# Kernel tuning notes

Measured on AMD Instinct MI355X. Metric: run time of the kernel, lower is better.

The kernel has to match this reference:

```python
import jax, jax.numpy as jnp
import numpy as np
import math

B, S, DIM, QK, HID = 20, 500, 300, 128, 600  # batch, seq, model dim, query_key_dim, hidden_dim
ROT = 32          # rotary dim = min(32, query_key_dim)
NB, MD = 32, 128  # T5 bias num_buckets, max_distance


def _layernorm(x, g, b, eps=1e-5):
    mu = jnp.mean(x, axis=-1, keepdims=True)
    var = jnp.var(x, axis=-1, keepdims=True)
    return (x - mu) / jnp.sqrt(var + eps) * g + b


def _rowquant(y, axis):
    # per-row (or per-col) symmetric int4-range quant used by the module:
    # scale = max|y|/15, clamp to [-15,15], truncate toward zero (torch .to(int8))
    s = jnp.max(jnp.abs(y), axis=axis, keepdims=True) / 15.0
    yq = jnp.trunc(jnp.clip(y / s, -15.0, 15.0))
    return yq, s


def _rotary(t):
    # rotary-embedding-torch: rotate first ROT features, interleaved pairs
    inv_freq = 1.0 / (10000.0 ** (jnp.arange(0, ROT, 2, dtype=jnp.float32) / ROT))  # [ROT/2]
    pos = jnp.arange(S, dtype=jnp.float32)
    freqs = jnp.repeat(pos[:, None] * inv_freq[None, :], 2, axis=-1)  # [S, ROT]
    cos, sin = jnp.cos(freqs), jnp.sin(freqs)
    tr, tp = t[..., :ROT], t[..., ROT:]
    x1, x2 = tr[..., 0::2], tr[..., 1::2]
    rot_half = jnp.stack([-x2, x1], axis=-1).reshape(tr.shape)
    return jnp.concatenate([tr * cos + rot_half * sin, tp], axis=-1)


def _t5_bias(rel_emb):
    # non-causal T5 relative position bucket, num_buckets=32 -> halved to 16
    pos = jnp.arange(S)
    n = -(pos[None, :] - pos[:, None])  # -(k_pos - q_pos)
    nb = NB // 2
    ret = (n < 0).astype(jnp.int32) * nb
    n = jnp.abs(n)
    max_exact = nb // 2
    is_small = n < max_exact
    n_safe = jnp.maximum(n, 1).astype(jnp.float32)
    val_large = max_exact + (jnp.log(n_safe / max_exact) / math.log(MD / max_exact) * (nb - max_exact)).astype(jnp.int32)
    val_large = jnp.minimum(val_large, nb - 1)
    bucket = ret + jnp.where(is_small, n, val_large)  # [S, S]
    return rel_emb[bucket, 0] * math.sqrt(QK)


def setup_inputs() -> dict:
    key = jax.random.key(0)
    ks = jax.random.split(key, 16)
    nrm = lambda i, shp, std=0.02: jax.random.normal(ks[i], shp, jnp.float32) * std
    uni = lambda i, shp, lo, hi: jax.random.uniform(ks[i], shp, jnp.float32, lo, hi)
    return {
        "x": jax.random.normal(ks[0], (B, S, DIM), jnp.float32),
        "norm_gamma": jnp.ones((DIM,), jnp.float32),
        "norm_beta": jnp.zeros((DIM,), jnp.float32),
        "Wh": nrm(1, (2 * HID, DIM)),
        "bh": jnp.zeros((2 * HID,), jnp.float32),
        "Wqk": nrm(2, (QK, DIM)),
        "bqk": jnp.zeros((QK,), jnp.float32),
        "os_gamma": nrm(3, (2, QK)),
        "os_beta": jnp.zeros((2, QK), jnp.float32),
        "Wo": nrm(4, (DIM, HID)),
        "bo": jnp.zeros((DIM,), jnp.float32),
        "rel_emb": nrm(5, (NB, 1), 0.1),
        "qk_s": uni(6, (DIM,), 0.5, 1.5),
        "hidden_s": uni(7, (DIM,), 0.5, 1.5),
        "out_s": uni(8, (HID,), 0.5, 1.5),
        "hidden_params": uni(9, (2 * HID,), 0.01, 0.05),
        "qk_params": uni(10, (QK,), 0.01, 0.05),
        "out_params": uni(11, (DIM,), 0.01, 0.05),
    }


def reference(x, norm_gamma, norm_beta, Wh, bh, Wqk, bqk, os_gamma, os_beta, Wo, bo,
              rel_emb, qk_s, hidden_s, out_s, hidden_params, qk_params, out_params):
    normed = _layernorm(x, norm_gamma, norm_beta)
    # token shift on first half of features
    half = DIM // 2
    x_shift = jnp.pad(normed[..., :half], ((0, 0), (1, 0), (0, 0)))[:, :S, :]
    normed = jnp.concatenate([x_shift, normed[..., half:]], axis=-1)

    # per-weight-column pre-scale then per-row int8 quant
    xq_q, sq = _rowquant(normed / qk_s, axis=-1)      # sq [B,S,1]
    xh_q, sh = _rowquant(normed / hidden_s, axis=-1)  # sh [B,S,1]

    # to_hidden: Linear + SiLU, then dequant outer(row_scale, hidden_params)
    v_gate = jax.nn.silu(xh_q @ Wh.T + bh) * (sh * hidden_params)  # [B,S,2*HID]
    v, gate = v_gate[..., :HID], v_gate[..., HID:]

    qk = jax.nn.silu(xq_q @ Wqk.T + bqk) * (sq * qk_params)  # [B,S,QK]
    q = qk * os_gamma[0] + os_beta[0]
    k = qk * os_gamma[1] + os_beta[1]
    q, k = _rotary(q), _rotary(k)

    qq, qs = _rowquant(q, axis=-1)
    kq, ks_ = _rowquant(k, axis=-1)
    sim = jnp.trunc(jnp.einsum('bid,bjd->bij', qq, kq)) * qs * jnp.swapaxes(ks_, 1, 2)
    sim = sim + _t5_bias(rel_emb)

    attn = jnp.square(jax.nn.relu(sim / S))
    aq, as_ = _rowquant(attn, axis=-1)  # as_ [B,S,1]
    vq, vs = _rowquant(v, axis=1)       # vs [B,1,HID] (per-column)
    out = jnp.trunc(jnp.einsum('bij,bjd->bid', aq, vq)) * as_ * vs  # [B,S,HID]

    out = out * gate / out_s
    oq, osc = _rowquant(out, axis=-1)
    out = (oq @ Wo.T + bo) * (osc * out_params)  # [B,S,DIM]
    return out + x
```

## Files before the change

kernel.cpp:

```cpp
#include <hip/hip_runtime.h>
#include <math.h>

#define B_   20
#define S_   500
#define DIM_ 300
#define QK_  128
#define HID_ 600
#define NROW (B_ * S_)

typedef int   v4i  __attribute__((ext_vector_type(4)));

__device__ __forceinline__ unsigned short f32_to_bf16(float f) {
  unsigned int u = __float_as_uint(f);
  unsigned int r = (u + 0x7FFFu + ((u >> 16) & 1u)) >> 16;
  return (unsigned short)r;
}
__device__ __forceinline__ float bf16_to_f32(unsigned short s) {
  return __uint_as_float(((unsigned int)s) << 16);
}

__device__ __forceinline__ float quant15(float y, float s) {
  return truncf(fminf(fmaxf(__fdiv_rn(y, s), -15.f), 15.f));
}

__global__ __launch_bounds__(64) void k_prep(
    const float* __restrict__ rel_emb, float* __restrict__ dbias,
    const float* __restrict__ Wh, signed char* __restrict__ q1h, float* __restrict__ s1h,
    const float* __restrict__ Wo, signed char* __restrict__ q1o,
    signed char* __restrict__ q2o, float* __restrict__ s1o, float* __restrict__ s2o,
    const float* __restrict__ Wqk, signed char* __restrict__ q1k,
    signed char* __restrict__ q2k, float* __restrict__ s1k, float* __restrict__ s2k) {
  __shared__ float red[64];
  int blk = blockIdx.x;
  int tid = threadIdx.x;
  if (blk < 16) {
    int idx = blk * 64 + tid;
    int dd = idx - 512;
    int ret = (dd < 0) ? 16 : 0;
    int n = dd < 0 ? -dd : dd;
    int v;
    if (n < 8)       v = n;
    else if (n < 12) v = 8;
    else if (n < 16) v = 9;
    else if (n < 23) v = 10;
    else if (n < 32) v = 11;
    else if (n < 46) v = 12;
    else if (n < 64) v = 13;
    else if (n < 91) v = 14;
    else             v = 15;
    dbias[idx] = __fmul_rn(rel_emb[ret + v], 11.313708498984761f);
    return;
  }
  const float* src; signed char* q1; signed char* q2; float* s1; float* s2;
  int j, R, C, CP;
  bool twolevel;
  if (blk < 1296) {
    j = blk - 16;  src = Wh;  q1 = q1h; q2 = 0; s1 = s1h; s2 = 0;
    R = 2 * HID_; C = DIM_; CP = 320; twolevel = false;
  } else if (blk < 1616) {
    j = blk - 1296; src = Wo; q1 = q1o; q2 = q2o; s1 = s1o; s2 = s2o;
    R = DIM_; C = HID_; CP = 640; twolevel = true;
  } else {
    j = blk - 1616; src = Wqk; q1 = q1k; q2 = q2k; s1 = s1k; s2 = s2k;
    R = QK_; C = DIM_; CP = 320; twolevel = true;
  }
  float m = 0.f;
  if (j < R)
    for (int k = tid; k < C; k += 64) m = fmaxf(m, fabsf(src[(size_t)j * C + k]));
  red[tid] = m; __syncthreads();
  for (int off = 32; off > 0; off >>= 1) {
    if (tid < off) red[tid] = fmaxf(red[tid], red[tid + off]);
    __syncthreads();
  }
  float s1v = red[0] / 127.0f;
  float s1inv = s1v > 0.f ? 1.0f / s1v : 0.f;
  if (!twolevel) {
    if (tid == 0) s1[j] = s1v;
    for (int k = tid; k < CP; k += 64) {
      float wv = (j < R && k < C) ? src[(size_t)j * C + k] : 0.f;
      float q1f = fminf(fmaxf(rintf(wv * s1inv), -127.f), 127.f);
      q1[(size_t)j * CP + k] = (signed char)q1f;
    }
    return;
  }
  __syncthreads();
  float mr = 0.f;
  if (j < R)
    for (int k = tid; k < C; k += 64) {
      float wv = src[(size_t)j * C + k];
      float q = fminf(fmaxf(rintf(wv * s1inv), -127.f), 127.f);
      mr = fmaxf(mr, fabsf(wv - s1v * q));
    }
  red[tid] = mr; __syncthreads();
  for (int off = 32; off > 0; off >>= 1) {
    if (tid < off) red[tid] = fmaxf(red[tid], red[tid + off]);
    __syncthreads();
  }
  float s2v = red[0] / 127.0f;
  float s2inv = s2v > 0.f ? 1.0f / s2v : 0.f;
  if (tid == 0) { s1[j] = s1v; s2[j] = s2v; }
  for (int k = tid; k < CP; k += 64) {
    float wv = (j < R && k < C) ? src[(size_t)j * C + k] : 0.f;
    float q1f = fminf(fmaxf(rintf(wv * s1inv), -127.f), 127.f);
    float rs = wv - s1v * q1f;
    float q2f = fminf(fmaxf(rintf(rs * s2inv), -127.f), 127.f);
    q1[(size_t)j * CP + k] = (signed char)q1f;
    q2[(size_t)j * CP + k] = (signed char)q2f;
  }
}

__global__ __launch_bounds__(256) void k_lnshift(
    const float* __restrict__ x,
    const float* __restrict__ g, const float* __restrict__ b,
    const float* __restrict__ qk_s, const float* __restrict__ hidden_s,
    signed char* __restrict__ xq8, signed char* __restrict__ xh8,
    float* __restrict__ sq, float* __restrict__ sh) {
  int lane = threadIdx.x & 63;
  int row = blockIdx.x * 4 + (threadIdx.x >> 6);
  if (row >= NROW) return;
  bool hasp = (row % S_) > 0;
  const float* xr = x + (size_t)row * DIM_;
  const float* xpr = x + (size_t)(row - 1) * DIM_;
  float xc[5], xp[5];
  #pragma unroll
  for (int i = 0; i < 5; ++i) {
    int c = lane + i * 64;
    xc[i] = (c < DIM_) ? xr[c] : 0.f;
    xp[i] = (hasp && c < DIM_) ? xpr[c] : 0.f;
  }
  float sc = 0.f, sp = 0.f;
  #pragma unroll
  for (int i = 0; i < 5; ++i) { sc += xc[i]; sp += xp[i]; }
  #pragma unroll
  for (int off = 1; off < 64; off <<= 1) {
    sc += __shfl_xor(sc, off);
    sp += __shfl_xor(sp, off);
  }
  float mu_c = sc / (float)DIM_, mu_p = sp / (float)DIM_;
  float vc = 0.f, vp = 0.f;
  #pragma unroll
  for (int i = 0; i < 5; ++i) {
    int c = lane + i * 64;
    if (c < DIM_) {
      float dc = xc[i] - mu_c; vc += dc * dc;
      float dp = xp[i] - mu_p; vp += dp * dp;
    }
  }
  #pragma unroll
  for (int off = 1; off < 64; off <<= 1) {
    vc += __shfl_xor(vc, off);
    vp += __shfl_xor(vp, off);
  }
  float den_c = sqrtf(vc / (float)DIM_ + 1e-5f);
  float den_p = sqrtf(vp / (float)DIM_ + 1e-5f);
  float yq[5], yh[5];
  float mq = 0.f, mh = 0.f;
  #pragma unroll
  for (int i = 0; i < 5; ++i) {
    int c = lane + i * 64;
    if (c < DIM_) {
      float src;
      if (c < DIM_ / 2)
        src = hasp ? __fdiv_rn(xp[i] - mu_p, den_p) * g[c] + b[c] : 0.f;
      else
        src = __fdiv_rn(xc[i] - mu_c, den_c) * g[c] + b[c];
      yq[i] = __fdiv_rn(src, qk_s[c]);
      yh[i] = __fdiv_rn(src, hidden_s[c]);
      mq = fmaxf(mq, fabsf(yq[i]));
      mh = fmaxf(mh, fabsf(yh[i]));
    }
  }
  #pragma unroll
  for (int off = 1; off < 64; off <<= 1) {
    mq = fmaxf(mq, __shfl_xor(mq, off));
    mh = fmaxf(mh, __shfl_xor(mh, off));
  }
  float sqv = mq / 15.0f, shv = mh / 15.0f;
  if (lane == 0) { sq[row] = sqv; sh[row] = shv; }
  #pragma unroll
  for (int i = 0; i < 5; ++i) {
    int c = lane + i * 64;
    if (c < DIM_) {
      xq8[(size_t)row * 320 + c] = (signed char)quant15(yq[i], sqv);
      xh8[(size_t)row * 320 + c] = (signed char)quant15(yh[i], shv);
    } else if (c < 320) {
      xq8[(size_t)row * 320 + c] = 0;
      xh8[(size_t)row * 320 + c] = 0;
    }
  }
}

__global__ __launch_bounds__(512) void k_hidden(
    const signed char* __restrict__ xh8p, const float* __restrict__ sh,
    const signed char* __restrict__ q1h, const float* __restrict__ s1h,
    const float* __restrict__ bh, const float* __restrict__ hp,
    unsigned short* __restrict__ v16, unsigned short* __restrict__ gate16,
    int* __restrict__ vsmax) {
  int i0 = blockIdx.y * 256;
  int j0 = blockIdx.x * 64;
  int tid = threadIdx.x;
  int w = tid >> 6, l = tid & 63, g = l >> 4, ln = l & 15;
  int wm = w >> 1, wn = w & 1;
  __shared__ __align__(16) signed char smem[33792];
  signed char* a_lds  = smem;
  signed char* b1_lds = smem + 16384;
  unsigned short* st  = (unsigned short*)smem;

  int r0 = tid >> 2, ch0 = tid & 3;
  int r1 = r0 + 128, ch1 = ch0;
  int koff0 = ((ch0 ^ ((r0 >> 1) & 3)) * 16);
  int koff1 = ((ch1 ^ ((r1 >> 1) & 3)) * 16);
  int ga0 = i0 + r0; if (ga0 >= NROW) ga0 = NROW - 1;
  int ga1 = i0 + r1; if (ga1 >= NROW) ga1 = NROW - 1;
  const signed char* srcA0 = xh8p + (size_t)ga0 * 320 + koff0;
  const signed char* srcA1 = xh8p + (size_t)ga1 * 320 + koff1;
  bool hasB = tid < 256;
  int br = (tid & 255) >> 2, bch = tid & 3;
  int bkoff = ((bch ^ ((br >> 1) & 3)) * 16);
  const signed char* srcB = q1h + (size_t)(j0 + br) * 320 + bkoff;

  v4i pa0 = *(const v4i*)srcA0;
  v4i pa1 = *(const v4i*)srcA1;
  v4i zero = {0, 0, 0, 0};
  v4i pb = hasB ? *(const v4i*)srcB : zero;

  int rxor = ((g ^ ((ln >> 1) & 3)) * 16);
  v4i acc1[4][2];
  #pragma unroll
  for (int sl = 0; sl < 4; ++sl)
    #pragma unroll
    for (int t = 0; t < 2; ++t) acc1[sl][t] = zero;

  for (int st_i = 0; st_i < 5; ++st_i) {
    *(v4i*)(a_lds + tid * 16)        = pa0;
    *(v4i*)(a_lds + 8192 + tid * 16) = pa1;
    if (hasB) *(v4i*)(b1_lds + tid * 16) = pb;
    __syncthreads();
    if (st_i < 4) {
      int k0 = (st_i + 1) * 64;
      pa0 = *(const v4i*)(srcA0 + k0);
      pa1 = *(const v4i*)(srcA1 + k0);
      if (hasB) pb = *(const v4i*)(srcB + k0);
    }
    v4i af[4];
    #pragma unroll
    for (int sl = 0; sl < 4; ++sl)
      af[sl] = *(const v4i*)(a_lds + (wm * 64 + sl * 16 + ln) * 64 + rxor);
    #pragma unroll
    for (int t = 0; t < 2; ++t) {
      int boff = (wn * 32 + t * 16 + ln) * 64 + rxor;
      v4i b1 = *(const v4i*)(b1_lds + boff);
      #pragma unroll
      for (int sl = 0; sl < 4; ++sl)
        acc1[sl][t] = __builtin_amdgcn_mfma_i32_16x16x64_i8(af[sl], b1, acc1[sl][t], 0, 0, 0);
    }
    __syncthreads();
  }
  int rbase = i0 + wm * 64;
  int b0 = rbase / S_;
  int bbound = (b0 + 1) * S_;
  int rtop = rbase + 63; if (rtop >= NROW) rtop = NROW - 1;
  int b1i = rtop / S_;
  #pragma unroll
  for (int t = 0; t < 2; ++t) {
    int col = j0 + wn * 32 + t * 16 + ln;
    int cl = wn * 32 + t * 16 + ln;
    if (col < 2 * HID_) {
      float s1v = s1h[col], bc = bh[col], hpc = hp[col];
      bool isv = col < HID_;
      float m0 = 0.f, m1 = 0.f;
      #pragma unroll
      for (int sl = 0; sl < 4; ++sl) {
        #pragma unroll
        for (int r = 0; r < 4; ++r) {
          int grow = rbase + sl * 16 + g * 4 + r;
          if (grow < NROW) {
            float z = s1v * (float)acc1[sl][t][r] + bc;
            float sig = 1.0f / (1.0f + __expf(-z));
            float val = __fmul_rn(z * sig, __fmul_rn(sh[grow], hpc));
            unsigned short hv = f32_to_bf16(val);
            st[(wm * 64 + sl * 16 + g * 4 + r) * 66 + cl] = hv;
            if (isv) {
              float vr = fabsf(bf16_to_f32(hv));
              if (grow < bbound) m0 = fmaxf(m0, vr);
              else               m1 = fmaxf(m1, vr);
            }
          }
        }
      }
      if (isv) {
        atomicMax(&vsmax[b0 * 640 + col], __float_as_int(m0));
        if (b1i != b0) atomicMax(&vsmax[b1i * 640 + col], __float_as_int(m1));
      }
    }
  }
  __syncthreads();
  for (int idx = tid; idx < 2048; idx += 512) {
    int r = idx >> 3, seg = idx & 7;
    int grow = i0 + r;
    int col0 = j0 + seg * 8;
    if (grow < NROW && col0 < 2 * HID_) {
      const unsigned int* sp = (const unsigned int*)(st + r * 66 + seg * 8);
      v4i pk;
      pk[0] = sp[0]; pk[1] = sp[1]; pk[2] = sp[2]; pk[3] = sp[3];
      if (col0 < HID_)
        *(v4i*)(v16 + (size_t)grow * HID_ + col0) = pk;
      else
        *(v4i*)(gate16 + (size_t)grow * HID_ + (col0 - HID_)) = pk;
    }
  }
}

__global__ __launch_bounds__(256) void k_qk(
    const signed char* __restrict__ xq8p, const float* __restrict__ sq,
    const signed char* __restrict__ q1k, const signed char* __restrict__ q2k,
    const float* __restrict__ s1k, const float* __restrict__ s2k,
    const float* __restrict__ bqk, const float* __restrict__ qkp,
    const float* __restrict__ osg, const float* __restrict__ osb,
    signed char* __restrict__ qq8, signed char* __restrict__ kq2,
    float* __restrict__ qs, float* __restrict__ ks) {
  int i0 = blockIdx.x * 64;
  int tid = threadIdx.x;
  int w = tid >> 6, l = tid & 63, g = l >> 4, ln = l & 15;
  __shared__ __align__(16) signed char a_lds[64 * 64];
  __shared__ __align__(16) signed char b1_lds[128 * 64];
  __shared__ __align__(16) signed char b2_lds[128 * 64];
  __shared__ float freqs[32];
  if (tid < 32) {
    double e = (double)(tid & ~1) / 32.0;
    freqs[tid] = (float)(1.0 / pow(10000.0, e));
  }
  int arow = tid >> 2;
  int xorb = (((tid & 3) ^ ((tid >> 3) & 3)) * 16);
  int ga = i0 + arow; if (ga >= NROW) ga = NROW - 1;
  const signed char* srcA   = xq8p + (size_t)ga * 320 + xorb;
  const signed char* srcB1a = q1k + (size_t)arow * 320 + xorb;
  const signed char* srcB1b = q1k + (size_t)(64 + arow) * 320 + xorb;
  const signed char* srcB2a = q2k + (size_t)arow * 320 + xorb;
  const signed char* srcB2b = q2k + (size_t)(64 + arow) * 320 + xorb;
  v4i pa   = *(const v4i*)srcA;
  v4i pb1a = *(const v4i*)srcB1a, pb1b = *(const v4i*)srcB1b;
  v4i pb2a = *(const v4i*)srcB2a, pb2b = *(const v4i*)srcB2b;
  int rxor = ((g ^ ((ln >> 1) & 3)) * 16);
  v4i acc1[8], acc2[8];
  v4i zero = {0, 0, 0, 0};
  #pragma unroll
  for (int t = 0; t < 8; ++t) { acc1[t] = zero; acc2[t] = zero; }
  for (int st = 0; st < 5; ++st) {
    *(v4i*)(a_lds + tid * 16)         = pa;
    *(v4i*)(b1_lds + tid * 16)        = pb1a;
    *(v4i*)(b1_lds + 4096 + tid * 16) = pb1b;
    *(v4i*)(b2_lds + tid * 16)        = pb2a;
    *(v4i*)(b2_lds + 4096 + tid * 16) = pb2b;
    __syncthreads();
    if (st < 4) {
      int k0 = (st + 1) * 64;
      pa   = *(const v4i*)(srcA + k0);
      pb1a = *(const v4i*)(srcB1a + k0);
      pb1b = *(const v4i*)(srcB1b + k0);
      pb2a = *(const v4i*)(srcB2a + k0);
      pb2b = *(const v4i*)(srcB2b + k0);
    }
    v4i af = *(const v4i*)(a_lds + (w * 16 + ln) * 64 + rxor);
    #pragma unroll
    for (int t = 0; t < 8; ++t) {
      int boff = (t * 16 + ln) * 64 + rxor;
      v4i b1 = *(const v4i*)(b1_lds + boff);
      v4i b2 = *(const v4i*)(b2_lds + boff);
      acc1[t] = __builtin_amdgcn_mfma_i32_16x16x64_i8(af, b1, acc1[t], 0, 0, 0);
      acc2[t] = __builtin_amdgcn_mfma_i32_16x16x64_i8(af, b2, acc2[t], 0, 0, 0);
    }
    __syncthreads();
  }
  int growr[4]; float sqr[4];
  #pragma unroll
  for (int r = 0; r < 4; ++r) {
    growr[r] = i0 + w * 16 + g * 4 + r;
    int gc = growr[r] < NROW ? growr[r] : NROW - 1;
    sqr[r] = sq[gc];
  }
  float qv[8][4], kv[8][4];
  #pragma unroll
  for (int t = 0; t < 8; ++t) {
    int c = t * 16 + ln;
    float s1v = s1k[c], s2v = s2k[c], bc = bqk[c], qkpc = qkp[c];
    float g0 = osg[c], g1 = osg[QK_ + c], b0 = osb[c], b1v = osb[QK_ + c];
    #pragma unroll
    for (int r = 0; r < 4; ++r) {
      float z = s1v * (float)acc1[t][r] + s2v * (float)acc2[t][r] + bc;
      float sig = 1.0f / (1.0f + expf(-z));
      float qkv = __fmul_rn(z * sig, __fmul_rn(sqr[r], qkpc));
      qv[t][r] = __fadd_rn(__fmul_rn(qkv, g0), b0);
      kv[t][r] = __fadd_rn(__fmul_rn(qkv, g1), b1v);
    }
  }
  #pragma unroll
  for (int t = 0; t < 2; ++t) {
    float inv = freqs[t * 16 + ln];
    #pragma unroll
    for (int r = 0; r < 4; ++r) {
      int pos = growr[r] % S_;
      float fr = __fmul_rn((float)pos, inv);
      float cs = cosf(fr), sn = sinf(fr);
      float qo = __shfl_xor(qv[t][r], 1);
      float ko = __shfl_xor(kv[t][r], 1);
      float rq = ((ln & 1) == 0) ? -qo : qo;
      float rk = ((ln & 1) == 0) ? -ko : ko;
      qv[t][r] = __fadd_rn(__fmul_rn(qv[t][r], cs), __fmul_rn(rq, sn));
      kv[t][r] = __fadd_rn(__fmul_rn(kv[t][r], cs), __fmul_rn(rk, sn));
    }
  }
  float qsv[4], ksv[4];
  #pragma unroll
  for (int r = 0; r < 4; ++r) {
    float mq = 0.f, mk = 0.f;
    #pragma unroll
    for (int t = 0; t < 8; ++t) {
      mq = fmaxf(mq, fabsf(qv[t][r]));
      mk = fmaxf(mk, fabsf(kv[t][r]));
    }
    #pragma unroll
    for (int off = 1; off < 16; off <<= 1) {
      mq = fmaxf(mq, __shfl_xor(mq, off));
      mk = fmaxf(mk, __shfl_xor(mk, off));
    }
    qsv[r] = mq / 15.0f; ksv[r] = mk / 15.0f;
    if (ln == 0 && growr[r] < NROW) { qs[growr[r]] = qsv[r]; ks[growr[r]] = ksv[r]; }
  }
  #pragma unroll
  for (int t = 0; t < 8; ++t) {
    int c = t * 16 + ln;
    #pragma unroll
    for (int r = 0; r < 4; ++r) {
      if (growr[r] < NROW) {
        qq8[(size_t)growr[r] * QK_ + c] = (signed char)quant15(qv[t][r], qsv[r]);
        int bb = growr[r] / S_, ss = growr[r] % S_;
        kq2[(((size_t)bb * 2 + (c >> 6)) * 512 + ss) * 64 + (c & 63)] =
            (signed char)quant15(kv[t][r], ksv[r]);
      }
    }
  }
}

__global__ __launch_bounds__(512) void k_simpv(
    const signed char* __restrict__ qq8, const signed char* __restrict__ kq2,
    const float* __restrict__ qs, const float* __restrict__ ks,
    const float* __restrict__ dbias,
    const signed char* __restrict__ vqt2, const float* __restrict__ vg,
    const unsigned short* __restrict__ gate16,
    signed char* __restrict__ oq8, float* __restrict__ osc) {
  int i0 = blockIdx.x * 16;
  int b = blockIdx.y;
  int tid = threadIdx.x;
  int w = tid >> 6, l = tid & 63, g = l >> 4, ln = l & 15;
  __shared__ __align__(16) signed char q_lds[16 * 144];
  __shared__ __align__(16) signed char p_lds[16 * 528];
  __shared__ float db[1024];
  __shared__ int rowmax[16];
  if (tid < 128) {
    int r = tid >> 3, ww = tid & 7;
    *(v4i*)(q_lds + r * 144 + ww * 16) =
        *(const v4i*)(qq8 + ((size_t)(b * S_ + i0 + r)) * QK_ + ww * 16);
  }
  for (int idx = tid; idx < 1024; idx += 512) db[idx] = dbias[idx];
  if (tid < 16) rowmax[tid] = 0;
  __syncthreads();
  v4i acc[4];
  v4i zero = {0, 0, 0, 0};
  #pragma unroll
  for (int t = 0; t < 4; ++t) acc[t] = zero;
  #pragma unroll
  for (int kk = 0; kk < 2; ++kk) {
    v4i afrag = *(const v4i*)(q_lds + ln * 144 + kk * 64 + g * 16);
    #pragma unroll
    for (int t = 0; t < 4; ++t) {
      int j0 = (w * 4 + t) * 16;
      v4i bfrag = *(const v4i*)(kq2 + (((size_t)b * 2 + kk) * 512 + j0 + ln) * 64 + g * 16);
      acc[t] = __builtin_amdgcn_mfma_i32_16x16x64_i8(afrag, bfrag, acc[t], 0, 0, 0);
    }
  }
  float qsr[4];
  #pragma unroll
  for (int r = 0; r < 4; ++r) qsr[r] = qs[b * S_ + i0 + g * 4 + r];
  float rm[4] = {0.f, 0.f, 0.f, 0.f};
  #pragma unroll
  for (int t = 0; t < 4; ++t) {
    int j = (w * 4 + t) * 16 + ln;
    bool jv = j < S_;
    float ksv = ks[b * S_ + j];
    #pragma unroll
    for (int r = 0; r < 4; ++r) {
      int ip = i0 + g * 4 + r;
      float av = 0.f;
      if (jv) {
        float simv = __fmul_rn(__fmul_rn((float)acc[t][r], qsr[r]), ksv);
        simv = __fadd_rn(simv, db[ip - j + 512]);
        float rr = fmaxf(__fmul_rn(simv, 0.002f), 0.f);
        av = __fmul_rn(rr, rr);
      }
      rm[r] = fmaxf(rm[r], av);
      acc[t][r] = __float_as_int(av);
    }
  }
  #pragma unroll
  for (int r = 0; r < 4; ++r) atomicMax(&rowmax[g * 4 + r], __float_as_int(rm[r]));
  __syncthreads();
  float asr[4], rinv[4];
  #pragma unroll
  for (int r = 0; r < 4; ++r) {
    asr[r] = __int_as_float(rowmax[g * 4 + r]) / 15.0f;
    rinv[r] = __fdiv_rn(1.0f, asr[r]);
  }
  #pragma unroll
  for (int t = 0; t < 4; ++t) {
    int j = (w * 4 + t) * 16 + ln;
    #pragma unroll
    for (int r = 0; r < 4; ++r) {
      float y = __int_as_float(acc[t][r]);
      float q = truncf(fminf(fmaxf(__fmul_rn(y, rinv[r]), -15.f), 15.f));
      p_lds[(g * 4 + r) * 528 + j] = (signed char)q;
    }
  }
  __syncthreads();
  if (tid < 16) rowmax[tid] = 0;
  __syncthreads();
  v4i pacc[5];
  #pragma unroll
  for (int t = 0; t < 5; ++t) pacc[t] = zero;
  for (int kk = 0; kk < 8; ++kk) {
    v4i afrag = *(const v4i*)(p_lds + ln * 528 + kk * 64 + g * 16);
    const signed char* bbase = vqt2 + (((size_t)b * 8 + kk) * 640) * 64 + g * 16;
    #pragma unroll
    for (int t = 0; t < 5; ++t) {
      int d = (w * 5 + t) * 16 + ln;
      v4i bfrag = *(const v4i*)(bbase + (size_t)d * 64);
      pacc[t] = __builtin_amdgcn_mfma_i32_16x16x64_i8(afrag, bfrag, pacc[t], 0, 0, 0);
    }
  }
  float rm2[4] = {0.f, 0.f, 0.f, 0.f};
  #pragma unroll
  for (int t = 0; t < 5; ++t) {
    int d = (w * 5 + t) * 16 + ln;
    bool dv = d < HID_;
    float vgv = vg[b * 640 + d];
    #pragma unroll
    for (int r = 0; r < 4; ++r) {
      float o = 0.f;
      if (dv) {
        float gt = bf16_to_f32(gate16[((size_t)(b * S_ + i0 + g * 4 + r)) * HID_ + d]);
        o = __fmul_rn(__fmul_rn(__fmul_rn((float)pacc[t][r], asr[r]), vgv), gt);
      }
      rm2[r] = fmaxf(rm2[r], fabsf(o));
      pacc[t][r] = __float_as_int(o);
    }
  }
  #pragma unroll
  for (int r = 0; r < 4; ++r) atomicMax(&rowmax[g * 4 + r], __float_as_int(rm2[r]));
  __syncthreads();
  float orinv[4];
  #pragma unroll
  for (int r = 0; r < 4; ++r) {
    float osr = __int_as_float(rowmax[g * 4 + r]) / 15.0f;
    orinv[r] = __fdiv_rn(1.0f, osr);
  }
  #pragma unroll
  for (int t = 0; t < 5; ++t) {
    int d = (w * 5 + t) * 16 + ln;
    #pragma unroll
    for (int r = 0; r < 4; ++r) {
      int il = i0 + g * 4 + r;
      if (il < S_) {
        signed char valc = 0;
        if (d < HID_) {
          float q = truncf(fminf(fmaxf(
              __fmul_rn(__int_as_float(pacc[t][r]), orinv[r]), -15.f), 15.f));
          valc = (signed char)q;
        }
        oq8[((size_t)b * S_ + il) * 640 + d] = valc;
      }
    }
  }
  if (tid < 16 && i0 + tid < S_)
    osc[b * S_ + i0 + tid] = __int_as_float(rowmax[tid]) / 15.0f;
}

__global__ __launch_bounds__(256) void k_vq2(const unsigned short* __restrict__ v16,
                                             const int* __restrict__ vsmax,
                                             const float* __restrict__ out_s,
                                             signed char* __restrict__ vqt2,
                                             float* __restrict__ vg) {
  int b = blockIdx.z;
  int s0 = blockIdx.x * 64;
  int d0 = blockIdx.y * 64;
  __shared__ float tile[64][65];
  int tid = threadIdx.x;
  int dj = tid & 63, si4 = tid >> 6;
  #pragma unroll
  for (int it = 0; it < 16; ++it) {
    int s = s0 + it * 4 + si4;
    int d = d0 + dj;
    float val = 0.f;
    if (s < S_ && d < HID_) val = bf16_to_f32(v16[((size_t)b * S_ + s) * HID_ + d]);
    tile[it * 4 + si4][dj] = val;
  }
  if (blockIdx.x == 0 && tid < 64) {
    int d = d0 + tid;
    float vsv = __int_as_float(vsmax[b * 640 + d]) / 15.0f;
    vg[b * 640 + d] = (d < HID_) ? __fdiv_rn(vsv, out_s[d]) : 0.f;
  }
  __syncthreads();
  int dd = tid >> 2, seg = tid & 3;
  int d = d0 + dd;
  int kk = s0 >> 6;
  v4i pack = {0, 0, 0, 0};
  if (d < HID_) {
    float vsv = __int_as_float(vsmax[b * 640 + d]) / 15.0f;
    signed char* pc = (signed char*)&pack;
    #pragma unroll
    for (int e = 0; e < 16; ++e)
      pc[e] = (signed char)quant15(tile[seg * 16 + e][dd], vsv);
  }
  *(v4i*)(vqt2 + ((((size_t)b * 8 + kk) * 640) + d) * 64 + seg * 16) = pack;
}

__global__ __launch_bounds__(256) void k_final(
    const signed char* __restrict__ oq8p, const float* __restrict__ osc,
    const signed char* __restrict__ q1o, const signed char* __restrict__ q2o,
    const float* __restrict__ s1o, const float* __restrict__ s2o,
    const float* __restrict__ bo, const float* __restrict__ op,
    const float* __restrict__ x, float* __restrict__ out) {
  int i0 = blockIdx.x * 128;
  int j0 = blockIdx.y * 64;
  int tid = threadIdx.x;
  int w = tid >> 6, l = tid & 63, g = l >> 4, ln = l & 15;
  int wm = w >> 1, wn = w & 1;
  __shared__ __align__(16) signed char a_lds[128 * 64];
  __shared__ __align__(16) signed char b1_lds[64 * 64];
  __shared__ __align__(16) signed char b2_lds[64 * 64];

  int arow0 = tid >> 2;
  int xorb = (((tid & 3) ^ ((tid >> 3) & 3)) * 16);
  int ga0 = i0 + arow0;       if (ga0 >= NROW) ga0 = NROW - 1;
  int ga1 = i0 + arow0 + 64;  if (ga1 >= NROW) ga1 = NROW - 1;
  int gcol = j0 + arow0;
  const signed char* srcA0 = oq8p + (size_t)ga0 * 640 + xorb;
  const signed char* srcA1 = oq8p + (size_t)ga1 * 640 + xorb;
  const signed char* srcB1 = q1o + (size_t)gcol * 640 + xorb;
  const signed char* srcB2 = q2o + (size_t)gcol * 640 + xorb;

  v4i pa0 = *(const v4i*)(srcA0);
  v4i pa1 = *(const v4i*)(srcA1);
  v4i pb1 = *(const v4i*)(srcB1);
  v4i pb2 = *(const v4i*)(srcB2);

  int rxor = ((g ^ ((ln >> 1) & 3)) * 16);
  v4i acc1[4][2], acc2[4][2];
  v4i zero = {0, 0, 0, 0};
  #pragma unroll
  for (int sl = 0; sl < 4; ++sl)
    #pragma unroll
    for (int t = 0; t < 2; ++t) { acc1[sl][t] = zero; acc2[sl][t] = zero; }

  for (int st = 0; st < 10; ++st) {
    *(v4i*)(a_lds + tid * 16)        = pa0;
    *(v4i*)(a_lds + 4096 + tid * 16) = pa1;
    *(v4i*)(b1_lds + tid * 16)       = pb1;
    *(v4i*)(b2_lds + tid * 16)       = pb2;
    __syncthreads();
    if (st < 9) {
      int k0 = (st + 1) * 64;
      pa0 = *(const v4i*)(srcA0 + k0);
      pa1 = *(const v4i*)(srcA1 + k0);
      pb1 = *(const v4i*)(srcB1 + k0);
      pb2 = *(const v4i*)(srcB2 + k0);
    }
    v4i af[4];
    #pragma unroll
    for (int sl = 0; sl < 4; ++sl)
      af[sl] = *(const v4i*)(a_lds + (wm * 64 + sl * 16 + ln) * 64 + rxor);
    #pragma unroll
    for (int t = 0; t < 2; ++t) {
      int boff = (wn * 32 + t * 16 + ln) * 64 + rxor;
      v4i b1 = *(const v4i*)(b1_lds + boff);
      v4i b2 = *(const v4i*)(b2_lds + boff);
      #pragma unroll
      for (int sl = 0; sl < 4; ++sl) {
        acc1[sl][t] = __builtin_amdgcn_mfma_i32_16x16x64_i8(af[sl], b1, acc1[sl][t], 0, 0, 0);
        acc2[sl][t] = __builtin_amdgcn_mfma_i32_16x16x64_i8(af[sl], b2, acc2[sl][t], 0, 0, 0);
      }
    }
    __syncthreads();
  }
  #pragma unroll
  for (int t = 0; t < 2; ++t) {
    int col = j0 + wn * 32 + t * 16 + ln;
    if (col < DIM_) {
      float s1v = s1o[col], s2v = s2o[col], bc = bo[col], opc = op[col];
      #pragma unroll
      for (int sl = 0; sl < 4; ++sl) {
        #pragma unroll
        for (int r = 0; r < 4; ++r) {
          int grow = i0 + wm * 64 + sl * 16 + g * 4 + r;
          if (grow < NROW) {
            float z = s1v * (float)acc1[sl][t][r] + s2v * (float)acc2[sl][t][r] + bc;
            float tval = __fmul_rn(osc[grow], opc);
            out[(size_t)grow * DIM_ + col] =
                __fmul_rn(z, tval) + x[(size_t)grow * DIM_ + col];
          }
        }
      }
    }
  }
}

extern "C" void kernel_launch(void* const* d_in, const int* in_sizes, int n_in,
                              void* d_out, int out_size, void* d_ws, size_t ws_size,
                              hipStream_t stream) {
  const float* x        = (const float*)d_in[0];
  const float* ng       = (const float*)d_in[1];
  const float* nbt      = (const float*)d_in[2];
  const float* Wh       = (const float*)d_in[3];
  const float* bh       = (const float*)d_in[4];
  const float* Wqk      = (const float*)d_in[5];
  const float* bqk      = (const float*)d_in[6];
  const float* osg      = (const float*)d_in[7];
  const float* osb      = (const float*)d_in[8];
  const float* Wo       = (const float*)d_in[9];
  const float* bo       = (const float*)d_in[10];
  const float* rel      = (const float*)d_in[11];
  const float* qk_s     = (const float*)d_in[12];
  const float* hidden_s = (const float*)d_in[13];
  const float* out_s    = (const float*)d_in[14];
  const float* hp       = (const float*)d_in[15];
  const float* qkp      = (const float*)d_in[16];
  const float* op       = (const float*)d_in[17];
  float* out = (float*)d_out;

  char* ws = (char*)d_ws;
  size_t off = 0;
  auto alloc = [&](size_t bytes) {
    void* p = ws + off;
    off += (bytes + 255) & ~(size_t)255;
    return p;
  };
  signed char* xq8    = (signed char*)alloc((size_t)(NROW + 128) * 320);
  signed char* xh8    = (signed char*)alloc((size_t)(NROW + 256) * 320);
  float*       sq     = (float*)      alloc((size_t)(NROW + 256) * 4);
  float*       sh     = (float*)      alloc((size_t)(NROW + 256) * 4);
  unsigned short* v16   = (unsigned short*)alloc((size_t)(NROW + 256) * HID_ * 2);
  unsigned short* gate16= (unsigned short*)alloc((size_t)(NROW + 256) * HID_ * 2);
  signed char* qq8    = (signed char*)alloc((size_t)(NROW + 64) * QK_);
  signed char* kq2    = (signed char*)alloc((size_t)B_ * 2 * 512 * 64);
  float*       qs     = (float*)      alloc((size_t)(NROW + 64) * 4);
  float*       ks     = (float*)      alloc((size_t)(NROW + 64) * 4);
  signed char* vqt2   = (signed char*)alloc((size_t)B_ * 8 * 640 * 64);
  float*       vg     = (float*)      alloc((size_t)B_ * 640 * 4);
  int*         vsmax  = (int*)        alloc((size_t)B_ * 640 * 4);
  signed char* oq8    = (signed char*)alloc((size_t)(NROW + 128) * 640);
  float*       osc    = (float*)      alloc((size_t)(NROW + 128) * 4);
  float*       dbias  = (float*)      alloc((size_t)1024 * 4);
  signed char* q1h    = (signed char*)alloc((size_t)1280 * 320);
  float*       s1h    = (float*)      alloc((size_t)1280 * 4);
  signed char* q1o    = (signed char*)alloc((size_t)320 * 640);
  signed char* q2o    = (signed char*)alloc((size_t)320 * 640);
  float*       s1o    = (float*)      alloc((size_t)320 * 4);
  float*       s2o    = (float*)      alloc((size_t)320 * 4);
  signed char* q1k    = (signed char*)alloc((size_t)QK_ * 320);
  signed char* q2k    = (signed char*)alloc((size_t)QK_ * 320);
  float*       s1k    = (float*)      alloc((size_t)QK_ * 4);
  float*       s2k    = (float*)      alloc((size_t)QK_ * 4);


  k_prep<<<1744, 64, 0, stream>>>(rel, dbias, Wh, q1h, s1h,
                                  Wo, q1o, q2o, s1o, s2o,
                                  Wqk, q1k, q2k, s1k, s2k);
  k_lnshift<<<(NROW + 3) / 4, 256, 0, stream>>>(x, ng, nbt, qk_s, hidden_s, xq8, xh8, sq, sh);
  k_hidden<<<dim3(19, 40), 512, 0, stream>>>(xh8, sh, q1h, s1h, bh, hp,
                                             v16, gate16, vsmax);
  k_qk<<<157, 256, 0, stream>>>(xq8, sq, q1k, q2k, s1k, s2k, bqk, qkp, osg, osb,
                                qq8, kq2, qs, ks);
  k_vq2<<<dim3(8, 10, B_), 256, 0, stream>>>(v16, vsmax, out_s, vqt2, vg);
  k_simpv<<<dim3(32, B_), 512, 0, stream>>>(qq8, kq2, qs, ks, dbias, vqt2, vg,
                                            gate16, oq8, osc);
  k_final<<<dim3(79, 5), 256, 0, stream>>>(oq8, osc, q1o, q2o, s1o, s2o, bo, op, x, out);
}
```

Baseline: 135.7 us.

## Fuse prep with layernorm, hidden with qk GEMM, and drop Wo residual quant

```diff
diff --git a/kernel.cpp b/kernel.cpp
--- a/kernel.cpp
+++ b/kernel.cpp
@@ -23,18 +23,99 @@
   return truncf(fminf(fmaxf(__fdiv_rn(y, s), -15.f), 15.f));
 }
 
-__global__ __launch_bounds__(64) void k_prep(
+__global__ __launch_bounds__(256) void k_prep_ln(
+    const float* __restrict__ x,
+    const float* __restrict__ g, const float* __restrict__ b,
+    const float* __restrict__ qk_s, const float* __restrict__ hidden_s,
+    signed char* __restrict__ xq8, signed char* __restrict__ xh8,
+    float* __restrict__ sq, float* __restrict__ sh,
     const float* __restrict__ rel_emb, float* __restrict__ dbias,
     const float* __restrict__ Wh, signed char* __restrict__ q1h, float* __restrict__ s1h,
-    const float* __restrict__ Wo, signed char* __restrict__ q1o,
-    signed char* __restrict__ q2o, float* __restrict__ s1o, float* __restrict__ s2o,
+    const float* __restrict__ Wo, signed char* __restrict__ q1o, float* __restrict__ s1o,
     const float* __restrict__ Wqk, signed char* __restrict__ q1k,
     signed char* __restrict__ q2k, float* __restrict__ s1k, float* __restrict__ s2k) {
-  __shared__ float red[64];
   int blk = blockIdx.x;
   int tid = threadIdx.x;
-  if (blk < 16) {
-    int idx = blk * 64 + tid;
+  int lane = tid & 63;
+  if (blk < 2500) {
+    int row = blk * 4 + (tid >> 6);
+    if (row >= NROW) return;
+    bool hasp = (row % S_) > 0;
+    const float* xr = x + (size_t)row * DIM_;
+    const float* xpr = x + (size_t)(row - 1) * DIM_;
+    float xc[5], xp[5];
+    #pragma unroll
+    for (int i = 0; i < 5; ++i) {
+      int c = lane + i * 64;
+      xc[i] = (c < DIM_) ? xr[c] : 0.f;
+      xp[i] = (hasp && c < DIM_) ? xpr[c] : 0.f;
+    }
+    float sc = 0.f, sp = 0.f;
+    #pragma unroll
+    for (int i = 0; i < 5; ++i) { sc += xc[i]; sp += xp[i]; }
+    #pragma unroll
+    for (int off = 1; off < 64; off <<= 1) {
+      sc += __shfl_xor(sc, off);
+      sp += __shfl_xor(sp, off);
+    }
+    float mu_c = sc / (float)DIM_, mu_p = sp / (float)DIM_;
+    float vc = 0.f, vp = 0.f;
+    #pragma unroll
+    for (int i = 0; i < 5; ++i) {
+      int c = lane + i * 64;
+      if (c < DIM_) {
+        float dc = xc[i] - mu_c; vc += dc * dc;
+        float dp = xp[i] - mu_p; vp += dp * dp;
+      }
+    }
+    #pragma unroll
+    for (int off = 1; off < 64; off <<= 1) {
+      vc += __shfl_xor(vc, off);
+      vp += __shfl_xor(vp, off);
+    }
+    float den_c = sqrtf(vc / (float)DIM_ + 1e-5f);
+    float den_p = sqrtf(vp / (float)DIM_ + 1e-5f);
+    float yq[5], yh[5];
+    float mq = 0.f, mh = 0.f;
+    #pragma unroll
+    for (int i = 0; i < 5; ++i) {
+      int c = lane + i * 64;
+      if (c < DIM_) {
+        float src;
+        if (c < DIM_ / 2)
+          src = hasp ? __fdiv_rn(xp[i] - mu_p, den_p) * g[c] + b[c] : 0.f;
+        else
+          src = __fdiv_rn(xc[i] - mu_c, den_c) * g[c] + b[c];
+        yq[i] = __fdiv_rn(src, qk_s[c]);
+        yh[i] = __fdiv_rn(src, hidden_s[c]);
+        mq = fmaxf(mq, fabsf(yq[i]));
+        mh = fmaxf(mh, fabsf(yh[i]));
+      }
+    }
+    #pragma unroll
+    for (int off = 1; off < 64; off <<= 1) {
+      mq = fmaxf(mq, __shfl_xor(mq, off));
+      mh = fmaxf(mh, __shfl_xor(mh, off));
+    }
+    float sqv = mq / 15.0f, shv = mh / 15.0f;
+    if (lane == 0) { sq[row] = sqv; sh[row] = shv; }
+    #pragma unroll
+    for (int i = 0; i < 5; ++i) {
+      int c = lane + i * 64;
+      if (c < DIM_) {
+        xq8[(size_t)row * 320 + c] = (signed char)quant15(yq[i], sqv);
+        xh8[(size_t)row * 320 + c] = (signed char)quant15(yh[i], shv);
+      } else if (c < 320) {
+        xq8[(size_t)row * 320 + c] = 0;
+        xh8[(size_t)row * 320 + c] = 0;
+      }
+    }
+    return;
+  }
+  int jidx = (blk - 2500) * 4 + (tid >> 6);
+  if (jidx >= 1744) return;
+  if (jidx < 16) {
+    int idx = jidx * 64 + lane;
     int dd = idx - 512;
     int ret = (dd < 0) ? 16 : 0;
     int n = dd < 0 ? -dd : dd;
@@ -51,392 +132,289 @@
     dbias[idx] = __fmul_rn(rel_emb[ret + v], 11.313708498984761f);
     return;
   }
-  const float* src; signed char* q1; signed char* q2; float* s1; float* s2;
-  int j, R, C, CP;
+  const float* src; signed char* q1; float* s1;
+  int j, C, CP;
   bool twolevel;
-  if (blk < 1296) {
-    j = blk - 16;  src = Wh;  q1 = q1h; q2 = 0; s1 = s1h; s2 = 0;
-    R = 2 * HID_; C = DIM_; CP = 320; twolevel = false;
-  } else if (blk < 1616) {
-    j = blk - 1296; src = Wo; q1 = q1o; q2 = q2o; s1 = s1o; s2 = s2o;
-    R = DIM_; C = HID_; CP = 640; twolevel = true;
-  } else {
-    j = blk - 1616; src = Wqk; q1 = q1k; q2 = q2k; s1 = s1k; s2 = s2k;
-    R = QK_; C = DIM_; CP = 320; twolevel = true;
-  }
+  if (jidx < 1296)      { j = jidx - 16;   src = Wh;  q1 = q1h; s1 = s1h; C = DIM_; CP = 320; twolevel = false; }
+  else if (jidx < 1616) { j = jidx - 1296; src = Wo;  q1 = q1o; s1 = s1o; C = HID_; CP = 640; twolevel = false; }
+  else                  { j = jidx - 1616; src = Wqk; q1 = q1k; s1 = s1k; C = DIM_; CP = 320; twolevel = true;  }
   float m = 0.f;
-  if (j < R)
-    for (int k = tid; k < C; k += 64) m = fmaxf(m, fabsf(src[(size_t)j * C + k]));
-  red[tid] = m; __syncthreads();
-  for (int off = 32; off > 0; off >>= 1) {
-    if (tid < off) red[tid] = fmaxf(red[tid], red[tid + off]);
-    __syncthreads();
-  }
-  float s1v = red[0] / 127.0f;
+  for (int k = lane; k < C; k += 64) m = fmaxf(m, fabsf(src[(size_t)j * C + k]));
+  #pragma unroll
+  for (int off = 1; off < 64; off <<= 1) m = fmaxf(m, __shfl_xor(m, off));
+  float s1v = m / 127.0f;
   float s1inv = s1v > 0.f ? 1.0f / s1v : 0.f;
   if (!twolevel) {
-    if (tid == 0) s1[j] = s1v;
-    for (int k = tid; k < CP; k += 64) {
-      float wv = (j < R && k < C) ? src[(size_t)j * C + k] : 0.f;
+    if (lane == 0) s1[j] = s1v;
+    for (int k = lane; k < CP; k += 64) {
+      float wv = (k < C) ? src[(size_t)j * C + k] : 0.f;
       float q1f = fminf(fmaxf(rintf(wv * s1inv), -127.f), 127.f);
       q1[(size_t)j * CP + k] = (signed char)q1f;
     }
     return;
   }
-  __syncthreads();
   float mr = 0.f;
-  if (j < R)
-    for (int k = tid; k < C; k += 64) {
-      float wv = src[(size_t)j * C + k];
-      float q = fminf(fmaxf(rintf(wv * s1inv), -127.f), 127.f);
-      mr = fmaxf(mr, fabsf(wv - s1v * q));
-    }
-  red[tid] = mr; __syncthreads();
-  for (int off = 32; off > 0; off >>= 1) {
-    if (tid < off) red[tid] = fmaxf(red[tid], red[tid + off]);
-    __syncthreads();
-  }
-  float s2v = red[0] / 127.0f;
+  for (int k = lane; k < C; k += 64) {
+    float wv = src[(size_t)j * C + k];
+    float q = fminf(fmaxf(rintf(wv * s1inv), -127.f), 127.f);
+    mr = fmaxf(mr, fabsf(wv - s1v * q));
+  }
+  #pragma unroll
+  for (int off = 1; off < 64; off <<= 1) mr = fmaxf(mr, __shfl_xor(mr, off));
+  float s2v = mr / 127.0f;
   float s2inv = s2v > 0.f ? 1.0f / s2v : 0.f;
-  if (tid == 0) { s1[j] = s1v; s2[j] = s2v; }
-  for (int k = tid; k < CP; k += 64) {
-    float wv = (j < R && k < C) ? src[(size_t)j * C + k] : 0.f;
+  if (lane == 0) { s1k[j] = s1v; s2k[j] = s2v; }
+  for (int k = lane; k < CP; k += 64) {
+    float wv = (k < C) ? src[(size_t)j * C + k] : 0.f;
     float q1f = fminf(fmaxf(rintf(wv * s1inv), -127.f), 127.f);
     float rs = wv - s1v * q1f;
     float q2f = fminf(fmaxf(rintf(rs * s2inv), -127.f), 127.f);
-    q1[(size_t)j * CP + k] = (signed char)q1f;
-    q2[(size_t)j * CP + k] = (signed char)q2f;
-  }
-}
-
-__global__ __launch_bounds__(256) void k_lnshift(
-    const float* __restrict__ x,
-    const float* __restrict__ g, const float* __restrict__ b,
-    const float* __restrict__ qk_s, const float* __restrict__ hidden_s,
-    signed char* __restrict__ xq8, signed char* __restrict__ xh8,
-    float* __restrict__ sq, float* __restrict__ sh) {
-  int lane = threadIdx.x & 63;
-  int row = blockIdx.x * 4 + (threadIdx.x >> 6);
-  if (row >= NROW) return;
-  bool hasp = (row % S_) > 0;
-  const float* xr = x + (size_t)row * DIM_;
-  const float* xpr = x + (size_t)(row - 1) * DIM_;
-  float xc[5], xp[5];
-  #pragma unroll
-  for (int i = 0; i < 5; ++i) {
-    int c = lane + i * 64;
-    xc[i] = (c < DIM_) ? xr[c] : 0.f;
-    xp[i] = (hasp && c < DIM_) ? xpr[c] : 0.f;
-  }
-  float sc = 0.f, sp = 0.f;
-  #pragma unroll
-  for (int i = 0; i < 5; ++i) { sc += xc[i]; sp += xp[i]; }
-  #pragma unroll
-  for (int off = 1; off < 64; off <<= 1) {
-    sc += __shfl_xor(sc, off);
-    sp += __shfl_xor(sp, off);
-  }
-  float mu_c = sc / (float)DIM_, mu_p = sp / (float)DIM_;
-  float vc = 0.f, vp = 0.f;
-  #pragma unroll
-  for (int i = 0; i < 5; ++i) {
-    int c = lane + i * 64;
-    if (c < DIM_) {
-      float dc = xc[i] - mu_c; vc += dc * dc;
-      float dp = xp[i] - mu_p; vp += dp * dp;
-    }
-  }
-  #pragma unroll
-  for (int off = 1; off < 64; off <<= 1) {
-    vc += __shfl_xor(vc, off);
-    vp += __shfl_xor(vp, off);
-  }
-  float den_c = sqrtf(vc / (float)DIM_ + 1e-5f);
-  float den_p = sqrtf(vp / (float)DIM_ + 1e-5f);
-  float yq[5], yh[5];
-  float mq = 0.f, mh = 0.f;
-  #pragma unroll
-  for (int i = 0; i < 5; ++i) {
-    int c = lane + i * 64;
-    if (c < DIM_) {
-      float src;
-      if (c < DIM_ / 2)
-        src = hasp ? __fdiv_rn(xp[i] - mu_p, den_p) * g[c] + b[c] : 0.f;
-      else
-        src = __fdiv_rn(xc[i] - mu_c, den_c) * g[c] + b[c];
-      yq[i] = __fdiv_rn(src, qk_s[c]);
-      yh[i] = __fdiv_rn(src, hidden_s[c]);
-      mq = fmaxf(mq, fabsf(yq[i]));
-      mh = fmaxf(mh, fabsf(yh[i]));
-    }
-  }
-  #pragma unroll
-  for (int off = 1; off < 64; off <<= 1) {
-    mq = fmaxf(mq, __shfl_xor(mq, off));
-    mh = fmaxf(mh, __shfl_xor(mh, off));
-  }
-  float sqv = mq / 15.0f, shv = mh / 15.0f;
-  if (lane == 0) { sq[row] = sqv; sh[row] = shv; }
-  #pragma unroll
-  for (int i = 0; i < 5; ++i) {
-    int c = lane + i * 64;
-    if (c < DIM_) {
-      xq8[(size_t)row * 320 + c] = (signed char)quant15(yq[i], sqv);
-      xh8[(size_t)row * 320 + c] = (signed char)quant15(yh[i], shv);
-    } else if (c < 320) {
-      xq8[(size_t)row * 320 + c] = 0;
-      xh8[(size_t)row * 320 + c] = 0;
-    }
-  }
-}
-
-__global__ __launch_bounds__(512) void k_hidden(
-    const signed char* __restrict__ xh8p, const float* __restrict__ sh,
+    q1k[(size_t)j * CP + k] = (signed char)q1f;
+    q2k[(size_t)j * CP + k] = (signed char)q2f;
+  }
+}
+
+__global__ __launch_bounds__(512) void k_hqk(
+    const signed char* __restrict__ xh8p, const signed char* __restrict__ xq8p,
+    const float* __restrict__ sh, const float* __restrict__ sq,
     const signed char* __restrict__ q1h, const float* __restrict__ s1h,
     const float* __restrict__ bh, const float* __restrict__ hp,
     unsigned short* __restrict__ v16, unsigned short* __restrict__ gate16,
-    int* __restrict__ vsmax) {
-  int i0 = blockIdx.y * 256;
-  int j0 = blockIdx.x * 64;
-  int tid = threadIdx.x;
-  int w = tid >> 6, l = tid & 63, g = l >> 4, ln = l & 15;
-  int wm = w >> 1, wn = w & 1;
-  __shared__ __align__(16) signed char smem[33792];
-  signed char* a_lds  = smem;
-  signed char* b1_lds = smem + 16384;
-  unsigned short* st  = (unsigned short*)smem;
-
-  int r0 = tid >> 2, ch0 = tid & 3;
-  int r1 = r0 + 128, ch1 = ch0;
-  int koff0 = ((ch0 ^ ((r0 >> 1) & 3)) * 16);
-  int koff1 = ((ch1 ^ ((r1 >> 1) & 3)) * 16);
-  int ga0 = i0 + r0; if (ga0 >= NROW) ga0 = NROW - 1;
-  int ga1 = i0 + r1; if (ga1 >= NROW) ga1 = NROW - 1;
-  const signed char* srcA0 = xh8p + (size_t)ga0 * 320 + koff0;
-  const signed char* srcA1 = xh8p + (size_t)ga1 * 320 + koff1;
-  bool hasB = tid < 256;
-  int br = (tid & 255) >> 2, bch = tid & 3;
-  int bkoff = ((bch ^ ((br >> 1) & 3)) * 16);
-  const signed char* srcB = q1h + (size_t)(j0 + br) * 320 + bkoff;
-
-  v4i pa0 = *(const v4i*)srcA0;
-  v4i pa1 = *(const v4i*)srcA1;
-  v4i zero = {0, 0, 0, 0};
-  v4i pb = hasB ? *(const v4i*)srcB : zero;
-
-  int rxor = ((g ^ ((ln >> 1) & 3)) * 16);
-  v4i acc1[4][2];
-  #pragma unroll
-  for (int sl = 0; sl < 4; ++sl)
-    #pragma unroll
-    for (int t = 0; t < 2; ++t) acc1[sl][t] = zero;
-
-  for (int st_i = 0; st_i < 5; ++st_i) {
-    *(v4i*)(a_lds + tid * 16)        = pa0;
-    *(v4i*)(a_lds + 8192 + tid * 16) = pa1;
-    if (hasB) *(v4i*)(b1_lds + tid * 16) = pb;
-    __syncthreads();
-    if (st_i < 4) {
-      int k0 = (st_i + 1) * 64;
-      pa0 = *(const v4i*)(srcA0 + k0);
-      pa1 = *(const v4i*)(srcA1 + k0);
-      if (hasB) pb = *(const v4i*)(srcB + k0);
-    }
-    v4i af[4];
-    #pragma unroll
-    for (int sl = 0; sl < 4; ++sl)
-      af[sl] = *(const v4i*)(a_lds + (wm * 64 + sl * 16 + ln) * 64 + rxor);
-    #pragma unroll
-    for (int t = 0; t < 2; ++t) {
-      int boff = (wn * 32 + t * 16 + ln) * 64 + rxor;
-      v4i b1 = *(const v4i*)(b1_lds + boff);
-      #pragma unroll
-      for (int sl = 0; sl < 4; ++sl)
-        acc1[sl][t] = __builtin_amdgcn_mfma_i32_16x16x64_i8(af[sl], b1, acc1[sl][t], 0, 0, 0);
-    }
-    __syncthreads();
-  }
-  int rbase = i0 + wm * 64;
-  int b0 = rbase / S_;
-  int bbound = (b0 + 1) * S_;
-  int rtop = rbase + 63; if (rtop >= NROW) rtop = NROW - 1;
-  int b1i = rtop / S_;
-  #pragma unroll
-  for (int t = 0; t < 2; ++t) {
-    int col = j0 + wn * 32 + t * 16 + ln;
-    int cl = wn * 32 + t * 16 + ln;
-    if (col < 2 * HID_) {
-      float s1v = s1h[col], bc = bh[col], hpc = hp[col];
-      bool isv = col < HID_;
-      float m0 = 0.f, m1 = 0.f;
-      #pragma unroll
-      for (int sl = 0; sl < 4; ++sl) {
-        #pragma unroll
-        for (int r = 0; r < 4; ++r) {
-          int grow = rbase + sl * 16 + g * 4 + r;
-          if (grow < NROW) {
-            float z = s1v * (float)acc1[sl][t][r] + bc;
-            float sig = 1.0f / (1.0f + __expf(-z));
-            float val = __fmul_rn(z * sig, __fmul_rn(sh[grow], hpc));
-            unsigned short hv = f32_to_bf16(val);
-            st[(wm * 64 + sl * 16 + g * 4 + r) * 66 + cl] = hv;
-            if (isv) {
-              float vr = fabsf(bf16_to_f32(hv));
-              if (grow < bbound) m0 = fmaxf(m0, vr);
-              else               m1 = fmaxf(m1, vr);
-            }
-          }
-        }
-      }
-      if (isv) {
-        atomicMax(&vsmax[b0 * 640 + col], __float_as_int(m0));
-        if (b1i != b0) atomicMax(&vsmax[b1i * 640 + col], __float_as_int(m1));
-      }
-    }
-  }
-  __syncthreads();
-  for (int idx = tid; idx < 2048; idx += 512) {
-    int r = idx >> 3, seg = idx & 7;
-    int grow = i0 + r;
-    int col0 = j0 + seg * 8;
-    if (grow < NROW && col0 < 2 * HID_) {
-      const unsigned int* sp = (const unsigned int*)(st + r * 66 + seg * 8);
-      v4i pk;
-      pk[0] = sp[0]; pk[1] = sp[1]; pk[2] = sp[2]; pk[3] = sp[3];
-      if (col0 < HID_)
-        *(v4i*)(v16 + (size_t)grow * HID_ + col0) = pk;
-      else
-        *(v4i*)(gate16 + (size_t)grow * HID_ + (col0 - HID_)) = pk;
-    }
-  }
-}
-
-__global__ __launch_bounds__(256) void k_qk(
-    const signed char* __restrict__ xq8p, const float* __restrict__ sq,
+    int* __restrict__ vsmax,
     const signed char* __restrict__ q1k, const signed char* __restrict__ q2k,
     const float* __restrict__ s1k, const float* __restrict__ s2k,
     const float* __restrict__ bqk, const float* __restrict__ qkp,
     const float* __restrict__ osg, const float* __restrict__ osb,
     signed char* __restrict__ qq8, signed char* __restrict__ kq2,
     float* __restrict__ qs, float* __restrict__ ks) {
-  int i0 = blockIdx.x * 64;
+  __shared__ __align__(16) signed char smem[33792];
+  int blk = blockIdx.x;
   int tid = threadIdx.x;
   int w = tid >> 6, l = tid & 63, g = l >> 4, ln = l & 15;
-  __shared__ __align__(16) signed char a_lds[64 * 64];
-  __shared__ __align__(16) signed char b1_lds[128 * 64];
-  __shared__ __align__(16) signed char b2_lds[128 * 64];
-  __shared__ float freqs[32];
-  if (tid < 32) {
-    double e = (double)(tid & ~1) / 32.0;
-    freqs[tid] = (float)(1.0 / pow(10000.0, e));
-  }
-  int arow = tid >> 2;
-  int xorb = (((tid & 3) ^ ((tid >> 3) & 3)) * 16);
-  int ga = i0 + arow; if (ga >= NROW) ga = NROW - 1;
-  const signed char* srcA   = xq8p + (size_t)ga * 320 + xorb;
-  const signed char* srcB1a = q1k + (size_t)arow * 320 + xorb;
-  const signed char* srcB1b = q1k + (size_t)(64 + arow) * 320 + xorb;
-  const signed char* srcB2a = q2k + (size_t)arow * 320 + xorb;
-  const signed char* srcB2b = q2k + (size_t)(64 + arow) * 320 + xorb;
-  v4i pa   = *(const v4i*)srcA;
-  v4i pb1a = *(const v4i*)srcB1a, pb1b = *(const v4i*)srcB1b;
-  v4i pb2a = *(const v4i*)srcB2a, pb2b = *(const v4i*)srcB2b;
+  v4i zero = {0, 0, 0, 0};
   int rxor = ((g ^ ((ln >> 1) & 3)) * 16);
-  v4i acc1[8], acc2[8];
-  v4i zero = {0, 0, 0, 0};
-  #pragma unroll
-  for (int t = 0; t < 8; ++t) { acc1[t] = zero; acc2[t] = zero; }
-  for (int st = 0; st < 5; ++st) {
-    *(v4i*)(a_lds + tid * 16)         = pa;
-    *(v4i*)(b1_lds + tid * 16)        = pb1a;
-    *(v4i*)(b1_lds + 4096 + tid * 16) = pb1b;
-    *(v4i*)(b2_lds + tid * 16)        = pb2a;
-    *(v4i*)(b2_lds + 4096 + tid * 16) = pb2b;
+
+  if (blk < 760) {
+    int j0 = (blk % 19) * 64;
+    int i0 = (blk / 19) * 256;
+    int wm = w >> 1, wn = w & 1;
+    signed char* a_lds  = smem;
+    signed char* b1_lds = smem + 16384;
+    unsigned short* st  = (unsigned short*)smem;
+
+    int r0 = tid >> 2, ch0 = tid & 3;
+    int r1 = r0 + 128;
+    int koff0 = ((ch0 ^ ((r0 >> 1) & 3)) * 16);
+    int koff1 = ((ch0 ^ ((r1 >> 1) & 3)) * 16);
+    int ga0 = i0 + r0; if (ga0 >= NROW) ga0 = NROW - 1;
+    int ga1 = i0 + r1; if (ga1 >= NROW) ga1 = NROW - 1;
+    const signed char* srcA0 = xh8p + (size_t)ga0 * 320 + koff0;
+    const signed char* srcA1 = xh8p + (size_t)ga1 * 320 + koff1;
+    bool hasB = tid < 256;
+    int br = (tid & 255) >> 2, bch = tid & 3;
+    int bkoff = ((bch ^ ((br >> 1) & 3)) * 16);
+    const signed char* srcB = q1h + (size_t)(j0 + br) * 320 + bkoff;
+
+    v4i pa0 = *(const v4i*)srcA0;
+    v4i pa1 = *(const v4i*)srcA1;
+    v4i pb = hasB ? *(const v4i*)srcB : zero;
+
+    v4i acc1[4][2];
+    #pragma unroll
+    for (int sl = 0; sl < 4; ++sl)
+      #pragma unroll
+      for (int t = 0; t < 2; ++t) acc1[sl][t] = zero;
+
+    for (int st_i = 0; st_i < 5; ++st_i) {
+      *(v4i*)(a_lds + tid * 16)        = pa0;
+      *(v4i*)(a_lds + 8192 + tid * 16) = pa1;
+      if (hasB) *(v4i*)(b1_lds + tid * 16) = pb;
+      __syncthreads();
+      if (st_i < 4) {
+        int k0 = (st_i + 1) * 64;
+        pa0 = *(const v4i*)(srcA0 + k0);
+        pa1 = *(const v4i*)(srcA1 + k0);
+        if (hasB) pb = *(const v4i*)(srcB + k0);
+      }
+      v4i af[4];
+      #pragma unroll
+      for (int sl = 0; sl < 4; ++sl)
+        af[sl] = *(const v4i*)(a_lds + (wm * 64 + sl * 16 + ln) * 64 + rxor);
+      #pragma unroll
+      for (int t = 0; t < 2; ++t) {
+        int boff = (wn * 32 + t * 16 + ln) * 64 + rxor;
+        v4i b1 = *(const v4i*)(b1_lds + boff);
+        #pragma unroll
+        for (int sl = 0; sl < 4; ++sl)
+          acc1[sl][t] = __builtin_amdgcn_mfma_i32_16x16x64_i8(af[sl], b1, acc1[sl][t], 0, 0, 0);
+      }
+      __syncthreads();
+    }
+    int rbase = i0 + wm * 64;
+    int b0 = rbase / S_;
+    int bbound = (b0 + 1) * S_;
+    int rtop = rbase + 63; if (rtop >= NROW) rtop = NROW - 1;
+    int b1i = rtop / S_;
+    #pragma unroll
+    for (int t = 0; t < 2; ++t) {
+      int col = j0 + wn * 32 + t * 16 + ln;
+      int cl = wn * 32 + t * 16 + ln;
+      if (col < 2 * HID_) {
+        float s1v = s1h[col], bc = bh[col], hpc = hp[col];
+        bool isv = col < HID_;
+        float m0 = 0.f, m1 = 0.f;
+        #pragma unroll
+        for (int sl = 0; sl < 4; ++sl) {
+          #pragma unroll
+          for (int r = 0; r < 4; ++r) {
+            int grow = rbase + sl * 16 + g * 4 + r;
+            if (grow < NROW) {
+              float z = s1v * (float)acc1[sl][t][r] + bc;
+              float sig = 1.0f / (1.0f + __expf(-z));
+              float val = __fmul_rn(z * sig, __fmul_rn(sh[grow], hpc));
+              unsigned short hv = f32_to_bf16(val);
+              st[(wm * 64 + sl * 16 + g * 4 + r) * 66 + cl] = hv;
+              if (isv) {
+                float vr = fabsf(bf16_to_f32(hv));
+                if (grow < bbound) m0 = fmaxf(m0, vr);
+                else               m1 = fmaxf(m1, vr);
+              }
+            }
+          }
+        }
+        if (isv) {
+          atomicMax(&vsmax[b0 * 640 + col], __float_as_int(m0));
+          if (b1i != b0) atomicMax(&vsmax[b1i * 640 + col], __float_as_int(m1));
+        }
+      }
+    }
     __syncthreads();
-    if (st < 4) {
-      int k0 = (st + 1) * 64;
-      pa   = *(const v4i*)(srcA + k0);
-      pb1a = *(const v4i*)(srcB1a + k0);
-      pb1b = *(const v4i*)(srcB1b + k0);
-      pb2a = *(const v4i*)(srcB2a + k0);
-      pb2b = *(const v4i*)(srcB2b + k0);
-    }
-    v4i af = *(const v4i*)(a_lds + (w * 16 + ln) * 64 + rxor);
+    for (int idx = tid; idx < 2048; idx += 512) {
+      int r = idx >> 3, seg = idx & 7;
+      int grow = i0 + r;
+      int col0 = j0 + seg * 8;
+      if (grow < NROW && col0 < 2 * HID_) {
+        const unsigned int* sp = (const unsigned int*)(st + r * 66 + seg * 8);
+        v4i pk;
+        pk[0] = sp[0]; pk[1] = sp[1]; pk[2] = sp[2]; pk[3] = sp[3];
+        if (col0 < HID_)
+          *(v4i*)(v16 + (size_t)grow * HID_ + col0) = pk;
+        else
+          *(v4i*)(gate16 + (size_t)grow * HID_ + (col0 - HID_)) = pk;
+      }
+    }
+    return;
+  }
+  {
+    int i0 = (blk - 760) * 128;
+    signed char* a_lds  = smem;
+    signed char* b1_lds = smem + 8192;
+    signed char* b2_lds = smem + 16384;
+    float* freqs = (float*)(smem + 24576);
+    if (tid < 32) {
+      double e = (double)(tid & ~1) / 32.0;
+      freqs[tid] = (float)(1.0 / pow(10000.0, e));
+    }
+    int r = tid >> 2, ch = tid & 3;
+    int koff = ((ch ^ ((r >> 1) & 3)) * 16);
+    int ga = i0 + r; if (ga >= NROW) ga = NROW - 1;
+    const signed char* srcA  = xq8p + (size_t)ga * 320 + koff;
+    const signed char* srcB1 = q1k + (size_t)r * 320 + koff;
+    const signed char* srcB2 = q2k + (size_t)r * 320 + koff;
+    v4i pa  = *(const v4i*)srcA;
+    v4i pb1 = *(const v4i*)srcB1;
+    v4i pb2 = *(const v4i*)srcB2;
+    v4i acc1[8], acc2[8];
+    #pragma unroll
+    for (int t = 0; t < 8; ++t) { acc1[t] = zero; acc2[t] = zero; }
+    for (int st = 0; st < 5; ++st) {
+      *(v4i*)(a_lds + tid * 16)  = pa;
+      *(v4i*)(b1_lds + tid * 16) = pb1;
+      *(v4i*)(b2_lds + tid * 16) = pb2;
+      __syncthreads();
+      if (st < 4) {
+        int k0 = (st + 1) * 64;
+        pa  = *(const v4i*)(srcA + k0);
+        pb1 = *(const v4i*)(srcB1 + k0);
+        pb2 = *(const v4i*)(srcB2 + k0);
+      }
+      v4i af = *(const v4i*)(a_lds + (w * 16 + ln) * 64 + rxor);
+      #pragma unroll
+      for (int t = 0; t < 8; ++t) {
+        int boff = (t * 16 + ln) * 64 + rxor;
+        v4i b1 = *(const v4i*)(b1_lds + boff);
+        v4i b2 = *(const v4i*)(b2_lds + boff);
+        acc1[t] = __builtin_amdgcn_mfma_i32_16x16x64_i8(af, b1, acc1[t], 0, 0, 0);
+        acc2[t] = __builtin_amdgcn_mfma_i32_16x16x64_i8(af, b2, acc2[t], 0, 0, 0);
+      }
+      __syncthreads();
+    }
+    int growr[4]; float sqr[4];
+    #pragma unroll
+    for (int r2 = 0; r2 < 4; ++r2) {
+      growr[r2] = i0 + w * 16 + g * 4 + r2;
+      int gc = growr[r2] < NROW ? growr[r2] : NROW - 1;
+      sqr[r2] = sq[gc];
+    }
+    float qv[8][4], kv[8][4];
     #pragma unroll
     for (int t = 0; t < 8; ++t) {
-      int boff = (t * 16 + ln) * 64 + rxor;
-      v4i b1 = *(const v4i*)(b1_lds + boff);
-      v4i b2 = *(const v4i*)(b2_lds + boff);
-      acc1[t] = __builtin_amdgcn_mfma_i32_16x16x64_i8(af, b1, acc1[t], 0, 0, 0);
-      acc2[t] = __builtin_amdgcn_mfma_i32_16x16x64_i8(af, b2, acc2[t], 0, 0, 0);
-    }
-    __syncthreads();
-  }
-  int growr[4]; float sqr[4];
-  #pragma unroll
-  for (int r = 0; r < 4; ++r) {
-    growr[r] = i0 + w * 16 + g * 4 + r;
-    int gc = growr[r] < NROW ? growr[r] : NROW - 1;
-    sqr[r] = sq[gc];
-  }
-  float qv[8][4], kv[8][4];
-  #pragma unroll
-  for (int t = 0; t < 8; ++t) {
-    int c = t * 16 + ln;
-    float s1v = s1k[c], s2v = s2k[c], bc = bqk[c], qkpc = qkp[c];
-    float g0 = osg[c], g1 = osg[QK_ + c], b0 = osb[c], b1v = osb[QK_ + c];
-    #pragma unroll
-    for (int r = 0; r < 4; ++r) {
-      float z = s1v * (float)acc1[t][r] + s2v * (float)acc2[t][r] + bc;
-      float sig = 1.0f / (1.0f + expf(-z));
-      float qkv = __fmul_rn(z * sig, __fmul_rn(sqr[r], qkpc));
-      qv[t][r] = __fadd_rn(__fmul_rn(qkv, g0), b0);
-      kv[t][r] = __fadd_rn(__fmul_rn(qkv, g1), b1v);
-    }
-  }
-  #pragma unroll
-  for (int t = 0; t < 2; ++t) {
-    float inv = freqs[t * 16 + ln];
-    #pragma unroll
-    for (int r = 0; r < 4; ++r) {
-      int pos = growr[r] % S_;
-      float fr = __fmul_rn((float)pos, inv);
-      float cs = cosf(fr), sn = sinf(fr);
-      float qo = __shfl_xor(qv[t][r], 1);
-      float ko = __shfl_xor(kv[t][r], 1);
-      float rq = ((ln & 1) == 0) ? -qo : qo;
-      float rk = ((ln & 1) == 0) ? -ko : ko;
-      qv[t][r] = __fadd_rn(__fmul_rn(qv[t][r], cs), __fmul_rn(rq, sn));
-      kv[t][r] = __fadd_rn(__fmul_rn(kv[t][r], cs), __fmul_rn(rk, sn));
-    }
-  }
-  float qsv[4], ksv[4];
-  #pragma unroll
-  for (int r = 0; r < 4; ++r) {
-    float mq = 0.f, mk = 0.f;
+      int c = t * 16 + ln;
+      float s1v = s1k[c], s2v = s2k[c], bc = bqk[c], qkpc = qkp[c];
+      float g0 = osg[c], g1 = osg[QK_ + c], b0 = osb[c], b1v = osb[QK_ + c];
+      #pragma unroll
+      for (int r2 = 0; r2 < 4; ++r2) {
+        float z = s1v * (float)acc1[t][r2] + s2v * (float)acc2[t][r2] + bc;
+        float sig = 1.0f / (1.0f + expf(-z));
+        float qkv = __fmul_rn(z * sig, __fmul_rn(sqr[r2], qkpc));
+        qv[t][r2] = __fadd_rn(__fmul_rn(qkv, g0), b0);
+        kv[t][r2] = __fadd_rn(__fmul_rn(qkv, g1), b1v);
+      }
+    }
+    #pragma unroll
+    for (int t = 0; t < 2; ++t) {
+      float inv = freqs[t * 16 + ln];
+      #pragma unroll
+      for (int r2 = 0; r2 < 4; ++r2) {
+        int pos = growr[r2] % S_;
+        float fr = __fmul_rn((float)pos, inv);
+        float cs = cosf(fr), sn = sinf(fr);
+        float qo = __shfl_xor(qv[t][r2], 1);
+        float ko = __shfl_xor(kv[t][r2], 1);
+        float rq = ((ln & 1) == 0) ? -qo : qo;
+        float rk = ((ln & 1) == 0) ? -ko : ko;
+        qv[t][r2] = __fadd_rn(__fmul_rn(qv[t][r2], cs), __fmul_rn(rq, sn));
+        kv[t][r2] = __fadd_rn(__fmul_rn(kv[t][r2], cs), __fmul_rn(rk, sn));
+      }
+    }
+    float qsv[4], ksv[4];
+    #pragma unroll
+    for (int r2 = 0; r2 < 4; ++r2) {
+      float mq = 0.f, mk = 0.f;
+      #pragma unroll
+      for (int t = 0; t < 8; ++t) {
+        mq = fmaxf(mq, fabsf(qv[t][r2]));
+        mk = fmaxf(mk, fabsf(kv[t][r2]));
+      }
+      #pragma unroll
+      for (int off = 1; off < 16; off <<= 1) {
+        mq = fmaxf(mq, __shfl_xor(mq, off));
+        mk = fmaxf(mk, __shfl_xor(mk, off));
+      }
+      qsv[r2] = mq / 15.0f; ksv[r2] = mk / 15.0f;
+      if (ln == 0 && growr[r2] < NROW) { qs[growr[r2]] = qsv[r2]; ks[growr[r2]] = ksv[r2]; }
+    }
     #pragma unroll
     for (int t = 0; t < 8; ++t) {
-      mq = fmaxf(mq, fabsf(qv[t][r]));
-      mk = fmaxf(mk, fabsf(kv[t][r]));
-    }
-    #pragma unroll
-    for (int off = 1; off < 16; off <<= 1) {
-      mq = fmaxf(mq, __shfl_xor(mq, off));
-      mk = fmaxf(mk, __shfl_xor(mk, off));
-    }
-    qsv[r] = mq / 15.0f; ksv[r] = mk / 15.0f;
-    if (ln == 0 && growr[r] < NROW) { qs[growr[r]] = qsv[r]; ks[growr[r]] = ksv[r]; }
-  }
-  #pragma unroll
-  for (int t = 0; t < 8; ++t) {
-    int c = t * 16 + ln;
-    #pragma unroll
-    for (int r = 0; r < 4; ++r) {
-      if (growr[r] < NROW) {
-        qq8[(size_t)growr[r] * QK_ + c] = (signed char)quant15(qv[t][r], qsv[r]);
-        int bb = growr[r] / S_, ss = growr[r] % S_;
-        kq2[(((size_t)bb * 2 + (c >> 6)) * 512 + ss) * 64 + (c & 63)] =
-            (signed char)quant15(kv[t][r], ksv[r]);
+      int c = t * 16 + ln;
+      #pragma unroll
+      for (int r2 = 0; r2 < 4; ++r2) {
+        if (growr[r2] < NROW) {
+          qq8[(size_t)growr[r2] * QK_ + c] = (signed char)quant15(qv[t][r2], qsv[r2]);
+          int bb = growr[r2] / S_, ss = growr[r2] % S_;
+          kq2[(((size_t)bb * 2 + (c >> 6)) * 512 + ss) * 64 + (c & 63)] =
+              (signed char)quant15(kv[t][r2], ksv[r2]);
+        }
       }
     }
   }
@@ -625,8 +603,7 @@
 
 __global__ __launch_bounds__(256) void k_final(
     const signed char* __restrict__ oq8p, const float* __restrict__ osc,
-    const signed char* __restrict__ q1o, const signed char* __restrict__ q2o,
-    const float* __restrict__ s1o, const float* __restrict__ s2o,
+    const signed char* __restrict__ q1o, const float* __restrict__ s1o,
     const float* __restrict__ bo, const float* __restrict__ op,
     const float* __restrict__ x, float* __restrict__ out) {
   int i0 = blockIdx.x * 128;
@@ -636,7 +613,6 @@
   int wm = w >> 1, wn = w & 1;
   __shared__ __align__(16) signed char a_lds[128 * 64];
   __shared__ __align__(16) signed char b1_lds[64 * 64];
-  __shared__ __align__(16) signed char b2_lds[64 * 64];
 
   int arow0 = tid >> 2;
   int xorb = (((tid & 3) ^ ((tid >> 3) & 3)) * 16);
@@ -646,33 +622,29 @@
   const signed char* srcA0 = oq8p + (size_t)ga0 * 640 + xorb;
   const signed char* srcA1 = oq8p + (size_t)ga1 * 640 + xorb;
   const signed char* srcB1 = q1o + (size_t)gcol * 640 + xorb;
-  const signed char* srcB2 = q2o + (size_t)gcol * 640 + xorb;
 
   v4i pa0 = *(const v4i*)(srcA0);
   v4i pa1 = *(const v4i*)(srcA1);
   v4i pb1 = *(const v4i*)(srcB1);
-  v4i pb2 = *(const v4i*)(srcB2);
 
   int rxor = ((g ^ ((ln >> 1) & 3)) * 16);
-  v4i acc1[4][2], acc2[4][2];
+  v4i acc1[4][2];
   v4i zero = {0, 0, 0, 0};
   #pragma unroll
   for (int sl = 0; sl < 4; ++sl)
     #pragma unroll
-    for (int t = 0; t < 2; ++t) { acc1[sl][t] = zero; acc2[sl][t] = zero; }
+    for (int t = 0; t < 2; ++t) acc1[sl][t] = zero;
 
   for (int st = 0; st < 10; ++st) {
     *(v4i*)(a_lds + tid * 16)        = pa0;
     *(v4i*)(a_lds + 4096 + tid * 16) = pa1;
     *(v4i*)(b1_lds + tid * 16)       = pb1;
-    *(v4i*)(b2_lds + tid * 16)       = pb2;
     __syncthreads();
     if (st < 9) {
       int k0 = (st + 1) * 64;
       pa0 = *(const v4i*)(srcA0 + k0);
       pa1 = *(const v4i*)(srcA1 + k0);
       pb1 = *(const v4i*)(srcB1 + k0);
-      pb2 = *(const v4i*)(srcB2 + k0);
     }
     v4i af[4];
     #pragma unroll
@@ -682,12 +654,9 @@
     for (int t = 0; t < 2; ++t) {
       int boff = (wn * 32 + t * 16 + ln) * 64 + rxor;
       v4i b1 = *(const v4i*)(b1_lds + boff);
-      v4i b2 = *(const v4i*)(b2_lds + boff);
-      #pragma unroll
-      for (int sl = 0; sl < 4; ++sl) {
+      #pragma unroll
+      for (int sl = 0; sl < 4; ++sl)
         acc1[sl][t] = __builtin_amdgcn_mfma_i32_16x16x64_i8(af[sl], b1, acc1[sl][t], 0, 0, 0);
-        acc2[sl][t] = __builtin_amdgcn_mfma_i32_16x16x64_i8(af[sl], b2, acc2[sl][t], 0, 0, 0);
-      }
     }
     __syncthreads();
   }
@@ -695,14 +664,14 @@
   for (int t = 0; t < 2; ++t) {
     int col = j0 + wn * 32 + t * 16 + ln;
     if (col < DIM_) {
-      float s1v = s1o[col], s2v = s2o[col], bc = bo[col], opc = op[col];
+      float s1v = s1o[col], bc = bo[col], opc = op[col];
       #pragma unroll
       for (int sl = 0; sl < 4; ++sl) {
         #pragma unroll
         for (int r = 0; r < 4; ++r) {
           int grow = i0 + wm * 64 + sl * 16 + g * 4 + r;
           if (grow < NROW) {
-            float z = s1v * (float)acc1[sl][t][r] + s2v * (float)acc2[sl][t][r] + bc;
+            float z = s1v * (float)acc1[sl][t][r] + bc;
             float tval = __fmul_rn(osc[grow], opc);
             out[(size_t)grow * DIM_ + col] =
                 __fmul_rn(z, tval) + x[(size_t)grow * DIM_ + col];
@@ -749,10 +718,10 @@
   float*       sh     = (float*)      alloc((size_t)(NROW + 256) * 4);
   unsigned short* v16   = (unsigned short*)alloc((size_t)(NROW + 256) * HID_ * 2);
   unsigned short* gate16= (unsigned short*)alloc((size_t)(NROW + 256) * HID_ * 2);
-  signed char* qq8    = (signed char*)alloc((size_t)(NROW + 64) * QK_);
+  signed char* qq8    = (signed char*)alloc((size_t)(NROW + 128) * QK_);
   signed char* kq2    = (signed char*)alloc((size_t)B_ * 2 * 512 * 64);
-  float*       qs     = (float*)      alloc((size_t)(NROW + 64) * 4);
-  float*       ks     = (float*)      alloc((size_t)(NROW + 64) * 4);
+  float*       qs     = (float*)      alloc((size_t)(NROW + 128) * 4);
+  float*       ks     = (float*)      alloc((size_t)(NROW + 128) * 4);
   signed char* vqt2   = (signed char*)alloc((size_t)B_ * 8 * 640 * 64);
   float*       vg     = (float*)      alloc((size_t)B_ * 640 * 4);
   int*         vsmax  = (int*)        alloc((size_t)B_ * 640 * 4);
@@ -762,25 +731,22 @@
   signed char* q1h    = (signed char*)alloc((size_t)1280 * 320);
   float*       s1h    = (float*)      alloc((size_t)1280 * 4);
   signed char* q1o    = (signed char*)alloc((size_t)320 * 640);
-  signed char* q2o    = (signed char*)alloc((size_t)320 * 640);
   float*       s1o    = (float*)      alloc((size_t)320 * 4);
-  float*       s2o    = (float*)      alloc((size_t)320 * 4);
   signed char* q1k    = (signed char*)alloc((size_t)QK_ * 320);
   signed char* q2k    = (signed char*)alloc((size_t)QK_ * 320);
   float*       s1k    = (float*)      alloc((size_t)QK_ * 4);
   float*       s2k    = (float*)      alloc((size_t)QK_ * 4);
 
 
-  k_prep<<<1744, 64, 0, stream>>>(rel, dbias, Wh, q1h, s1h,
-                                  Wo, q1o, q2o, s1o, s2o,
-                                  Wqk, q1k, q2k, s1k, s2k);
-  k_lnshift<<<(NROW + 3) / 4, 256, 0, stream>>>(x, ng, nbt, qk_s, hidden_s, xq8, xh8, sq, sh);
-  k_hidden<<<dim3(19, 40), 512, 0, stream>>>(xh8, sh, q1h, s1h, bh, hp,
-                                             v16, gate16, vsmax);
-  k_qk<<<157, 256, 0, stream>>>(xq8, sq, q1k, q2k, s1k, s2k, bqk, qkp, osg, osb,
-                                qq8, kq2, qs, ks);
+  k_prep_ln<<<2936, 256, 0, stream>>>(x, ng, nbt, qk_s, hidden_s, xq8, xh8, sq, sh,
+                                      rel, dbias, Wh, q1h, s1h, Wo, q1o, s1o,
+                                      Wqk, q1k, q2k, s1k, s2k);
+  k_hqk<<<839, 512, 0, stream>>>(xh8, xq8, sh, sq, q1h, s1h, bh, hp,
+                                 v16, gate16, vsmax,
+                                 q1k, q2k, s1k, s2k, bqk, qkp, osg, osb,
+                                 qq8, kq2, qs, ks);
   k_vq2<<<dim3(8, 10, B_), 256, 0, stream>>>(v16, vsmax, out_s, vqt2, vg);
   k_simpv<<<dim3(32, B_), 512, 0, stream>>>(qq8, kq2, qs, ks, dbias, vqt2, vg,
                                             gate16, oq8, osc);
-  k_final<<<dim3(79, 5), 256, 0, stream>>>(oq8, osc, q1o, q2o, s1o, s2o, bo, op, x, out);
-}
+  k_final<<<dim3(79, 5), 256, 0, stream>>>(oq8, osc, q1o, s1o, bo, op, x, out);
+}
```

After: 129.4 us. 4.6% less time.
